# Kernel optimization log

Hardware: AMD Instinct MI355X
Metric: run time of the kernel (lower is better)

Reference implementation:

```python
import jax, jax.numpy as jnp
import numpy as np

H, D = 12, 768
DH = D // H  # 64

def setup_inputs() -> dict:
    key = jax.random.key(0)
    ks = jax.random.split(key, 9)
    s = 0.02
    x  = jax.random.normal(ks[0], (8, 1024, D), dtype=jnp.float32)
    Wq = jax.random.normal(ks[1], (H, D, DH), dtype=jnp.float32) * s
    Wk = jax.random.normal(ks[2], (H, D, DH), dtype=jnp.float32) * s
    Wv = jax.random.normal(ks[3], (H, D, DH), dtype=jnp.float32) * s
    bq = jax.random.normal(ks[4], (H, DH), dtype=jnp.float32) * s
    bk = jax.random.normal(ks[5], (H, DH), dtype=jnp.float32) * s
    bv = jax.random.normal(ks[6], (H, DH), dtype=jnp.float32) * s
    Wo = jax.random.normal(ks[7], (D, D), dtype=jnp.float32) * s
    bo = jax.random.normal(ks[8], (D,), dtype=jnp.float32) * s
    return {"x": x, "Wq": Wq, "Wk": Wk, "Wv": Wv, "bq": bq, "bk": bk, "bv": bv, "Wo": Wo, "bo": bo}

def reference(x, Wq, Wk, Wv, bq, bk, bv, Wo, bo):
    # x: [B,S,D]; per-head projections batched over heads: [B,H,S,DH]
    q = jnp.einsum('bsd,hde->bhse', x, Wq) + bq[None, :, None, :]
    k = jnp.einsum('bsd,hde->bhse', x, Wk) + bk[None, :, None, :]
    v = jnp.einsum('bsd,hde->bhse', x, Wv) + bv[None, :, None, :]
    scores = jnp.einsum('bhse,bhte->bhst', q, k) / jnp.sqrt(jnp.float32(DH))
    probs = jax.nn.softmax(scores, axis=-1)  # dropout is identity (p=0 / eval)
    ctx = jnp.einsum('bhst,bhte->bhse', probs, v)  # [B,H,S,DH]
    B, _, S, _ = ctx.shape
    # concat heads along feature dim (head order matches torch cat order)
    ctx = jnp.transpose(ctx, (0, 2, 1, 3)).reshape(B, S, H * DH)
    out = jnp.einsum('bsd,de->bse', ctx, Wo) + bo
    return out
```

## Files before the change

kernel.cpp:

```cpp
#include <hip/hip_runtime.h>
#include <math.h>


constexpr int NB  = 8;
constexpr int SEQ = 1024;
constexpr int NH  = 12;
constexpr int DM  = 768;
constexpr int DHD = 64;
constexpr int MROWS = NB * SEQ;
constexpr int NQKV  = 3 * NH * DHD;

typedef __attribute__((ext_vector_type(8))) short short8;
typedef __attribute__((ext_vector_type(4))) float f32x4;

#define MFMA16(a,b,c) __builtin_amdgcn_mfma_f32_16x16x32_bf16((a),(b),(c),0,0,0)

#if __has_builtin(__builtin_amdgcn_exp2f)
#define EXP2(x) __builtin_amdgcn_exp2f(x)
#else
#define EXP2(x) exp2f(x)
#endif

__device__ __forceinline__ unsigned short f2bf(float f) {
    unsigned u = __float_as_uint(f);
    return (unsigned short)((u + 0x7fffu + ((u >> 16) & 1u)) >> 16);
}
__device__ __forceinline__ unsigned short f2bf_fast(float f) {
    return (unsigned short)((__float_as_uint(f) + 0x8000u) >> 16);
}

__device__ __forceinline__ void gl_lds16(const unsigned short* g, unsigned short* l) {
    __builtin_amdgcn_global_load_lds(
        (const __attribute__((address_space(1))) void*)g,
        (__attribute__((address_space(3))) void*)l, 16, 0, 0);
}

__device__ __forceinline__ void stageK(unsigned short* lds, const unsigned short* gbase,
                                       int i, int ln, int ldg) {
    int r    = i * 8 + (ln >> 3);
    int cpos = ln & 7;
    int cdat = (cpos - r) & 7;
    gl_lds16(gbase + (size_t)r * ldg + cdat * 8, lds + i * 512);
}
__device__ __forceinline__ short8 ldK(const unsigned short* buf, int row, int chunk) {
    int c = (chunk + row) & 7;
    return *(const short8*)&buf[row * 64 + c * 8];
}

__global__ __launch_bounds__(256) void prep_k(
    const float* __restrict__ x,
    const float* __restrict__ Wq, const float* __restrict__ Wk,
    const float* __restrict__ Wv, const float* __restrict__ Wo,
    unsigned short* __restrict__ xb, unsigned short* __restrict__ wt,
    unsigned short* __restrict__ wot) {
    __shared__ float tb[64][65];
    const int blk = blockIdx.x, tid = threadIdx.x;
    if (blk < 6144) {
        const int i = blk * 256 + tid;
        float4 v = ((const float4*)x)[i];
        ushort4 o;
        o.x = f2bf(v.x); o.y = f2bf(v.y); o.z = f2bf(v.z); o.w = f2bf(v.w);
        ((ushort4*)xb)[i] = o;
        return;
    }
    const int t = blk - 6144;
    const int job = t / 144, lb = t % 144;
    const float* W;
    unsigned short* dst;
    int C, r0, c0;
    if (job < 3) {
        const float* Ws = (job == 0) ? Wq : (job == 1 ? Wk : Wv);
        const int h = lb / 12, rb = lb % 12;
        W = Ws + (size_t)h * (DM * DHD);
        dst = wt + (size_t)(job * 12 + h) * (DM * DHD);
        C = DHD; r0 = rb * 64; c0 = 0;
    } else {
        W = Wo; dst = wot; C = DM;
        r0 = (lb / 12) * 64; c0 = (lb % 12) * 64;
    }
    const int rr = tid >> 2, cc = (tid & 3) * 16;
#pragma unroll
    for (int j = 0; j < 16; j += 4) {
        float4 v = *(const float4*)&W[(size_t)(r0 + rr) * C + c0 + cc + j];
        tb[rr][cc + j + 0] = v.x;
        tb[rr][cc + j + 1] = v.y;
        tb[rr][cc + j + 2] = v.z;
        tb[rr][cc + j + 3] = v.w;
    }
    __syncthreads();
#pragma unroll
    for (int j = 0; j < 16; ++j)
        dst[(size_t)(c0 + rr) * DM + r0 + cc + j] = f2bf(tb[cc + j][rr]);
}

__global__ __launch_bounds__(256, 3) void qkv_mfma_k(
    const unsigned short* __restrict__ xb, const unsigned short* __restrict__ wt,
    const float* __restrict__ bq, const float* __restrict__ bk, const float* __restrict__ bv,
    unsigned short* __restrict__ qb, unsigned short* __restrict__ kb,
    unsigned short* __restrict__ vT) {
    __shared__ unsigned short Ah[128 * 64], Bh[128 * 64];

    const int tid = threadIdx.x;
    const int wv = tid >> 6, ln = tid & 63, quad = ln >> 4, lnid = ln & 15;
    const int wvm = wv >> 1, wvn = wv & 1;
    const int row0 = blockIdx.x * 128, col0 = blockIdx.y * 128;
    const int sel = (col0 >= 2 * DM) ? 2 : (col0 >= DM ? 1 : 0);

    f32x4 acc[4][4];
#pragma unroll
    for (int i = 0; i < 4; ++i)
#pragma unroll
        for (int j = 0; j < 4; ++j) acc[i][j] = (f32x4){0.f, 0.f, 0.f, 0.f};

    const unsigned short* Ahg = xb + (size_t)row0 * DM;
    const unsigned short* Bhg = wt + (size_t)col0 * DM;
    constexpr int NIT = DM / 64;

    if (sel < 2) {
        for (int it = 0; it < NIT; ++it) {
            const int kc = it * 64;
            __syncthreads();
#pragma unroll
            for (int c = 0; c < 4; ++c) {
                stageK(Ah, Ahg + kc, wv * 4 + c, ln, DM);
                stageK(Bh, Bhg + kc, wv * 4 + c, ln, DM);
            }
            __syncthreads();
#pragma unroll
            for (int ks = 0; ks < 2; ++ks) {
                short8 a[4], b[4];
#pragma unroll
                for (int i = 0; i < 4; ++i)
                    a[i] = ldK(Ah, wvm * 64 + i * 16 + lnid, ks * 4 + quad);
#pragma unroll
                for (int j = 0; j < 4; ++j)
                    b[j] = ldK(Bh, wvn * 64 + j * 16 + lnid, ks * 4 + quad);
#pragma unroll
                for (int j = 0; j < 4; ++j)
#pragma unroll
                    for (int i = 0; i < 4; ++i)
                        acc[j][i] = MFMA16(b[j], a[i], acc[j][i]);
            }
        }
        const float scale = (sel == 0) ? 0.18033688011112042f : 1.0f;
        const float* bias = (sel == 0) ? bq : bk;
        unsigned short* oh = (sel == 0) ? qb : kb;
#pragma unroll
        for (int et = 0; et < 4; ++et) {
            const int e = col0 + wvn * 64 + et * 16 + quad * 4;
            const int he = e - sel * DM;
            const int hh2 = he >> 6, ee = he & 63;
            float4 bs = *(const float4*)&bias[he];
#pragma unroll
            for (int st = 0; st < 4; ++st) {
                const int srow = row0 + wvm * 64 + st * 16 + lnid;
                const int bb = srow >> 10, ss = srow & (SEQ - 1);
                ushort4 pk;
                pk.x = f2bf((acc[et][st][0] + bs.x) * scale);
                pk.y = f2bf((acc[et][st][1] + bs.y) * scale);
                pk.z = f2bf((acc[et][st][2] + bs.z) * scale);
                pk.w = f2bf((acc[et][st][3] + bs.w) * scale);
                *(ushort4*)&oh[((size_t)(bb * NH + hh2) * SEQ + ss) * DHD + ee] = pk;
            }
        }
    } else {
        for (int it = 0; it < NIT; ++it) {
            const int kc = it * 64;
            __syncthreads();
#pragma unroll
            for (int c = 0; c < 4; ++c) {
                stageK(Ah, Ahg + kc, wv * 4 + c, ln, DM);
                stageK(Bh, Bhg + kc, wv * 4 + c, ln, DM);
            }
            __syncthreads();
#pragma unroll
            for (int ks = 0; ks < 2; ++ks) {
                short8 a[4], b[4];
#pragma unroll
                for (int i = 0; i < 4; ++i)
                    a[i] = ldK(Ah, wvm * 64 + i * 16 + lnid, ks * 4 + quad);
#pragma unroll
                for (int j = 0; j < 4; ++j)
                    b[j] = ldK(Bh, wvn * 64 + j * 16 + lnid, ks * 4 + quad);
#pragma unroll
                for (int i = 0; i < 4; ++i)
#pragma unroll
                    for (int j = 0; j < 4; ++j)
                        acc[i][j] = MFMA16(a[i], b[j], acc[i][j]);
            }
        }
#pragma unroll
        for (int i = 0; i < 4; ++i) {
#pragma unroll
            for (int j = 0; j < 4; ++j) {
                const int col = col0 + wvn * 64 + j * 16 + lnid;
                const int he = col - 2 * DM;
                const int hh2 = he >> 6, ee = he & 63;
                const float bs = bv[he];
                const int srow = row0 + wvm * 64 + i * 16 + quad * 4;
                const int bb = srow >> 10, ss = srow & (SEQ - 1);
                ushort4 pk;
                pk.x = f2bf(acc[i][j][0] + bs);
                pk.y = f2bf(acc[i][j][1] + bs);
                pk.z = f2bf(acc[i][j][2] + bs);
                pk.w = f2bf(acc[i][j][3] + bs);
                *(ushort4*)&vT[((size_t)(bb * NH + hh2) * DHD + ee) * SEQ + ss] = pk;
            }
        }
    }
}

__global__ __launch_bounds__(512, 6) void attn_mfma_k(
    const unsigned short* __restrict__ qb, const unsigned short* __restrict__ kb,
    const unsigned short* __restrict__ vT, unsigned short* __restrict__ ctb) {
    __shared__ unsigned short ksh[2][64 * 64], vsm[2][64 * 64];
    __shared__ unsigned short ps[128 * 64];

    const int tid = threadIdx.x;
    const int wv = tid >> 6, ln = tid & 63, quad = ln >> 4, lnid = ln & 15;
    const int bhid = blockIdx.x % 96, qt = blockIdx.x / 96;
    const int b = bhid / NH, h = bhid % NH;
    const int q0 = qt * 128;
    const unsigned short* qhb = qb + (size_t)bhid * (SEQ * DHD);
    const unsigned short* khb = kb + (size_t)bhid * (SEQ * DHD);
    const unsigned short* vTb = vT + (size_t)bhid * (DHD * SEQ);

    const int prow = wv * 16 + lnid;

    short8 qf[2];
#pragma unroll
    for (int ks_ = 0; ks_ < 2; ++ks_)
        qf[ks_] = *(const short8*)(qhb + (size_t)(q0 + prow) * DHD + ks_ * 32 + quad * 8);

    f32x4 ctx[4];
#pragma unroll
    for (int j = 0; j < 4; ++j) ctx[j] = (f32x4){0.f, 0.f, 0.f, 0.f};
    float lsum = 0.f;

    stageK(ksh[0], khb, wv, ln, DHD);
    stageK(vsm[0], vTb, wv, ln, SEQ);

    for (int kt = 0; kt < SEQ / 64; ++kt) {
        const int cur = kt & 1;
        __syncthreads();
        if (kt + 1 < SEQ / 64) {
            stageK(ksh[cur ^ 1], khb + (kt + 1) * 64 * DHD, wv, ln, DHD);
            stageK(vsm[cur ^ 1], vTb + (kt + 1) * 64, wv, ln, SEQ);
        }

        f32x4 sc[4];
#pragma unroll
        for (int j = 0; j < 4; ++j) sc[j] = (f32x4){0.f, 0.f, 0.f, 0.f};
#pragma unroll
        for (int ks_ = 0; ks_ < 2; ++ks_) {
#pragma unroll
            for (int nt = 0; nt < 4; ++nt) {
                short8 kf = ldK(ksh[cur], nt * 16 + lnid, ks_ * 4 + quad);
                sc[nt] = MFMA16(kf, qf[ks_], sc[nt]);
            }
        }

#pragma unroll
        for (int nt = 0; nt < 4; ++nt) {
            float p0 = EXP2(sc[nt][0]);
            float p1 = EXP2(sc[nt][1]);
            float p2 = EXP2(sc[nt][2]);
            float p3 = EXP2(sc[nt][3]);
            lsum += (p0 + p1) + (p2 + p3);
            ushort4 pw;
            pw.x = f2bf_fast(p0);
            pw.y = f2bf_fast(p1);
            pw.z = f2bf_fast(p2);
            pw.w = f2bf_fast(p3);
            const int cpos = (2 * nt + (quad >> 1) + prow) & 7;
            *(ushort4*)&ps[prow * 64 + cpos * 8 + (quad & 1) * 4] = pw;
        }

#pragma unroll
        for (int kvs = 0; kvs < 2; ++kvs) {
            short8 pf = ldK(ps, prow, kvs * 4 + quad);
#pragma unroll
            for (int dt = 0; dt < 4; ++dt) {
                short8 vf = ldK(vsm[cur], dt * 16 + lnid, kvs * 4 + quad);
                ctx[dt] = MFMA16(vf, pf, ctx[dt]);
            }
        }
    }

    float s = lsum;
    s += __shfl_xor(s, 16, 64);
    s += __shfl_xor(s, 32, 64);
    const float inv = 1.0f / s;
    const int srow = b * SEQ + q0 + prow;
#pragma unroll
    for (int dt = 0; dt < 4; ++dt) {
        ushort4 pk;
        pk.x = f2bf(ctx[dt][0] * inv);
        pk.y = f2bf(ctx[dt][1] * inv);
        pk.z = f2bf(ctx[dt][2] * inv);
        pk.w = f2bf(ctx[dt][3] * inv);
        *(ushort4*)&ctb[(size_t)srow * DM + h * DHD + dt * 16 + quad * 4] = pk;
    }
}

__global__ __launch_bounds__(256, 3) void out_mfma_k(
    const unsigned short* __restrict__ ctb, const unsigned short* __restrict__ wot,
    const float* __restrict__ bo, float* __restrict__ out) {
    __shared__ unsigned short Ah[128 * 64], Bh[128 * 64];

    const int tid = threadIdx.x;
    const int wv = tid >> 6, ln = tid & 63, quad = ln >> 4, lnid = ln & 15;
    const int wvm = wv >> 1, wvn = wv & 1;
    const int row0 = blockIdx.x * 128, col0 = blockIdx.y * 128;

    f32x4 acc[4][4];
#pragma unroll
    for (int i = 0; i < 4; ++i)
#pragma unroll
        for (int j = 0; j < 4; ++j) acc[i][j] = (f32x4){0.f, 0.f, 0.f, 0.f};

    const unsigned short* Ahg = ctb + (size_t)row0 * DM;
    const unsigned short* Bhg = wot + (size_t)col0 * DM;

    constexpr int NIT = DM / 64;
    for (int it = 0; it < NIT; ++it) {
        const int kc = it * 64;
        __syncthreads();
#pragma unroll
        for (int c = 0; c < 4; ++c) {
            stageK(Ah, Ahg + kc, wv * 4 + c, ln, DM);
            stageK(Bh, Bhg + kc, wv * 4 + c, ln, DM);
        }
        __syncthreads();
#pragma unroll
        for (int ks = 0; ks < 2; ++ks) {
            short8 a[4], b[4];
#pragma unroll
            for (int i = 0; i < 4; ++i)
                a[i] = ldK(Ah, wvm * 64 + i * 16 + lnid, ks * 4 + quad);
#pragma unroll
            for (int j = 0; j < 4; ++j)
                b[j] = ldK(Bh, wvn * 64 + j * 16 + lnid, ks * 4 + quad);
#pragma unroll
            for (int j = 0; j < 4; ++j)
#pragma unroll
                for (int i = 0; i < 4; ++i)
                    acc[j][i] = MFMA16(b[j], a[i], acc[j][i]);
        }
    }

#pragma unroll
    for (int et = 0; et < 4; ++et) {
        const int colb = col0 + wvn * 64 + et * 16 + quad * 4;
        float4 bs = *(const float4*)&bo[colb];
#pragma unroll
        for (int st = 0; st < 4; ++st) {
            const int srow = row0 + wvm * 64 + st * 16 + lnid;
            float4 o;
            o.x = acc[et][st][0] + bs.x;
            o.y = acc[et][st][1] + bs.y;
            o.z = acc[et][st][2] + bs.z;
            o.w = acc[et][st][3] + bs.w;
            *(float4*)&out[(size_t)srow * DM + colb] = o;
        }
    }
}

extern "C" void kernel_launch(void* const* d_in, const int* in_sizes, int n_in,
                              void* d_out, int out_size, void* d_ws, size_t ws_size,
                              hipStream_t stream) {
    const float* x  = (const float*)d_in[0];
    const float* Wq = (const float*)d_in[1];
    const float* Wk = (const float*)d_in[2];
    const float* Wv = (const float*)d_in[3];
    const float* bq = (const float*)d_in[4];
    const float* bk = (const float*)d_in[5];
    const float* bv = (const float*)d_in[6];
    const float* Wo = (const float*)d_in[7];
    const float* bo = (const float*)d_in[8];
    float* out = (float*)d_out;

    char* w = (char*)d_ws;
    const size_t elsX = (size_t)MROWS * DM;
    const size_t elsQ = (size_t)NB * NH * SEQ * DHD;
    unsigned short* xb  = (unsigned short*)w;
    unsigned short* ctb = xb;
    size_t off = elsX * 2;
    unsigned short* wt  = (unsigned short*)(w + off); off += (size_t)NQKV * DM * 2;
    unsigned short* wot = (unsigned short*)(w + off); off += (size_t)DM * DM * 2;
    unsigned short* qbp = (unsigned short*)(w + off); off += elsQ * 2;
    unsigned short* kbp = (unsigned short*)(w + off); off += elsQ * 2;
    unsigned short* vTp = (unsigned short*)(w + off); off += elsQ * 2;

    prep_k<<<dim3(6144 + 576), 256, 0, stream>>>(x, Wq, Wk, Wv, Wo, xb, wt, wot);
    qkv_mfma_k<<<dim3(MROWS / 128, NQKV / 128), 256, 0, stream>>>(
        xb, wt, bq, bk, bv, qbp, kbp, vTp);
    attn_mfma_k<<<dim3(768), 512, 0, stream>>>(qbp, kbp, vTp, ctb);
    out_mfma_k<<<dim3(MROWS / 128, DM / 128), 256, 0, stream>>>(ctb, wot, bo, out);
}
```

Baseline: 190.1 us.

## Use 8-wave blocks in QKV GEMM and prefetch next K tile after fragment reads

The QKV projection kernel now runs 512 threads per block in a 2x4 wave grid, so each wave holds a 64x32 accumulator tile instead of 64x64. The main loop reads the A/B fragments for both k-substeps into registers first, then issues the global loads for the next K chunk into the same LDS buffers while the MFMAs run. This aims to hide global-load latency behind compute and to raise the number of waves per CU. In exchange each wave reuses less data from its fragments, and holding more fragments in registers may add register pressure.

```diff
diff --git a/kernel.cpp b/kernel.cpp
--- a/kernel.cpp
+++ b/kernel.cpp
@@ -93,7 +93,7 @@
         dst[(size_t)(c0 + rr) * DM + r0 + cc + j] = f2bf(tb[cc + j][rr]);
 }
 
-__global__ __launch_bounds__(256, 3) void qkv_mfma_k(
+__global__ __launch_bounds__(512, 4) void qkv_mfma_k(
     const unsigned short* __restrict__ xb, const unsigned short* __restrict__ wt,
     const float* __restrict__ bq, const float* __restrict__ bk, const float* __restrict__ bv,
     unsigned short* __restrict__ qb, unsigned short* __restrict__ kb,
@@ -102,98 +102,118 @@
 
     const int tid = threadIdx.x;
     const int wv = tid >> 6, ln = tid & 63, quad = ln >> 4, lnid = ln & 15;
-    const int wvm = wv >> 1, wvn = wv & 1;
+    const int wvm = wv >> 2, wvn = wv & 3;
     const int row0 = blockIdx.x * 128, col0 = blockIdx.y * 128;
     const int sel = (col0 >= 2 * DM) ? 2 : (col0 >= DM ? 1 : 0);
-
-    f32x4 acc[4][4];
-#pragma unroll
-    for (int i = 0; i < 4; ++i)
-#pragma unroll
-        for (int j = 0; j < 4; ++j) acc[i][j] = (f32x4){0.f, 0.f, 0.f, 0.f};
 
     const unsigned short* Ahg = xb + (size_t)row0 * DM;
     const unsigned short* Bhg = wt + (size_t)col0 * DM;
     constexpr int NIT = DM / 64;
 
+#pragma unroll
+    for (int c = 0; c < 2; ++c) {
+        stageK(Ah, Ahg, wv * 2 + c, ln, DM);
+        stageK(Bh, Bhg, wv * 2 + c, ln, DM);
+    }
+
     if (sel < 2) {
+        f32x4 acc[2][4];
+#pragma unroll
+        for (int j = 0; j < 2; ++j)
+#pragma unroll
+            for (int i = 0; i < 4; ++i) acc[j][i] = (f32x4){0.f, 0.f, 0.f, 0.f};
+
         for (int it = 0; it < NIT; ++it) {
-            const int kc = it * 64;
             __syncthreads();
-#pragma unroll
-            for (int c = 0; c < 4; ++c) {
-                stageK(Ah, Ahg + kc, wv * 4 + c, ln, DM);
-                stageK(Bh, Bhg + kc, wv * 4 + c, ln, DM);
+            short8 a[2][4], b[2][2];
+#pragma unroll
+            for (int ks = 0; ks < 2; ++ks) {
+#pragma unroll
+                for (int i = 0; i < 4; ++i)
+                    a[ks][i] = ldK(Ah, wvm * 64 + i * 16 + lnid, ks * 4 + quad);
+#pragma unroll
+                for (int j = 0; j < 2; ++j)
+                    b[ks][j] = ldK(Bh, wvn * 32 + j * 16 + lnid, ks * 4 + quad);
             }
             __syncthreads();
-#pragma unroll
-            for (int ks = 0; ks < 2; ++ks) {
-                short8 a[4], b[4];
-#pragma unroll
-                for (int i = 0; i < 4; ++i)
-                    a[i] = ldK(Ah, wvm * 64 + i * 16 + lnid, ks * 4 + quad);
-#pragma unroll
-                for (int j = 0; j < 4; ++j)
-                    b[j] = ldK(Bh, wvn * 64 + j * 16 + lnid, ks * 4 + quad);
-#pragma unroll
-                for (int j = 0; j < 4; ++j)
+            if (it + 1 < NIT) {
+                const int kc = (it + 1) * 64;
+#pragma unroll
+                for (int c = 0; c < 2; ++c) {
+                    stageK(Ah, Ahg + kc, wv * 2 + c, ln, DM);
+                    stageK(Bh, Bhg + kc, wv * 2 + c, ln, DM);
+                }
+            }
+#pragma unroll
+            for (int ks = 0; ks < 2; ++ks)
+#pragma unroll
+                for (int j = 0; j < 2; ++j)
 #pragma unroll
                     for (int i = 0; i < 4; ++i)
-                        acc[j][i] = MFMA16(b[j], a[i], acc[j][i]);
-            }
+                        acc[j][i] = MFMA16(b[ks][j], a[ks][i], acc[j][i]);
         }
         const float scale = (sel == 0) ? 0.18033688011112042f : 1.0f;
         const float* bias = (sel == 0) ? bq : bk;
         unsigned short* oh = (sel == 0) ? qb : kb;
 #pragma unroll
-        for (int et = 0; et < 4; ++et) {
-            const int e = col0 + wvn * 64 + et * 16 + quad * 4;
+        for (int jt = 0; jt < 2; ++jt) {
+            const int e = col0 + wvn * 32 + jt * 16 + quad * 4;
             const int he = e - sel * DM;
             const int hh2 = he >> 6, ee = he & 63;
             float4 bs = *(const float4*)&bias[he];
 #pragma unroll
-            for (int st = 0; st < 4; ++st) {
-                const int srow = row0 + wvm * 64 + st * 16 + lnid;
+            for (int it = 0; it < 4; ++it) {
+                const int srow = row0 + wvm * 64 + it * 16 + lnid;
                 const int bb = srow >> 10, ss = srow & (SEQ - 1);
                 ushort4 pk;
-                pk.x = f2bf((acc[et][st][0] + bs.x) * scale);
-                pk.y = f2bf((acc[et][st][1] + bs.y) * scale);
-                pk.z = f2bf((acc[et][st][2] + bs.z) * scale);
-                pk.w = f2bf((acc[et][st][3] + bs.w) * scale);
+                pk.x = f2bf((acc[jt][it][0] + bs.x) * scale);
+                pk.y = f2bf((acc[jt][it][1] + bs.y) * scale);
+                pk.z = f2bf((acc[jt][it][2] + bs.z) * scale);
+                pk.w = f2bf((acc[jt][it][3] + bs.w) * scale);
                 *(ushort4*)&oh[((size_t)(bb * NH + hh2) * SEQ + ss) * DHD + ee] = pk;
             }
         }
     } else {
+        f32x4 acc[4][2];
+#pragma unroll
+        for (int i = 0; i < 4; ++i)
+#pragma unroll
+            for (int j = 0; j < 2; ++j) acc[i][j] = (f32x4){0.f, 0.f, 0.f, 0.f};
+
         for (int it = 0; it < NIT; ++it) {
-            const int kc = it * 64;
             __syncthreads();
-#pragma unroll
-            for (int c = 0; c < 4; ++c) {
-                stageK(Ah, Ahg + kc, wv * 4 + c, ln, DM);
-                stageK(Bh, Bhg + kc, wv * 4 + c, ln, DM);
+            short8 a[2][4], b[2][2];
+#pragma unroll
+            for (int ks = 0; ks < 2; ++ks) {
+#pragma unroll
+                for (int i = 0; i < 4; ++i)
+                    a[ks][i] = ldK(Ah, wvm * 64 + i * 16 + lnid, ks * 4 + quad);
+#pragma unroll
+                for (int j = 0; j < 2; ++j)
+                    b[ks][j] = ldK(Bh, wvn * 32 + j * 16 + lnid, ks * 4 + quad);
             }
             __syncthreads();
-#pragma unroll
-            for (int ks = 0; ks < 2; ++ks) {
-                short8 a[4], b[4];
+            if (it + 1 < NIT) {
+                const int kc = (it + 1) * 64;
+#pragma unroll
+                for (int c = 0; c < 2; ++c) {
+                    stageK(Ah, Ahg + kc, wv * 2 + c, ln, DM);
+                    stageK(Bh, Bhg + kc, wv * 2 + c, ln, DM);
+                }
+            }
+#pragma unroll
+            for (int ks = 0; ks < 2; ++ks)
 #pragma unroll
                 for (int i = 0; i < 4; ++i)
-                    a[i] = ldK(Ah, wvm * 64 + i * 16 + lnid, ks * 4 + quad);
-#pragma unroll
-                for (int j = 0; j < 4; ++j)
-                    b[j] = ldK(Bh, wvn * 64 + j * 16 + lnid, ks * 4 + quad);
-#pragma unroll
-                for (int i = 0; i < 4; ++i)
-#pragma unroll
-                    for (int j = 0; j < 4; ++j)
-                        acc[i][j] = MFMA16(a[i], b[j], acc[i][j]);
-            }
+#pragma unroll
+                    for (int j = 0; j < 2; ++j)
+                        acc[i][j] = MFMA16(a[ks][i], b[ks][j], acc[i][j]);
         }
 #pragma unroll
         for (int i = 0; i < 4; ++i) {
 #pragma unroll
-            for (int j = 0; j < 4; ++j) {
-                const int col = col0 + wvn * 64 + j * 16 + lnid;
+            for (int j = 0; j < 2; ++j) {
+                const int col = col0 + wvn * 32 + j * 16 + lnid;
                 const int he = col - 2 * DM;
                 const int hh2 = he >> 6, ee = he & 63;
                 const float bs = bv[he];
@@ -393,7 +413,7 @@
     unsigned short* vTp = (unsigned short*)(w + off); off += elsQ * 2;
 
     prep_k<<<dim3(6144 + 576), 256, 0, stream>>>(x, Wq, Wk, Wv, Wo, xb, wt, wot);
-    qkv_mfma_k<<<dim3(MROWS / 128, NQKV / 128), 256, 0, stream>>>(
+    qkv_mfma_k<<<dim3(MROWS / 128, NQKV / 128), 512, 0, stream>>>(
         xb, wt, bq, bk, bv, qbp, kbp, vTp);
     attn_mfma_k<<<dim3(768), 512, 0, stream>>>(qbp, kbp, vTp, ctb);
     out_mfma_k<<<dim3(MROWS / 128, DM / 128), 256, 0, stream>>>(ctb, wot, bo, out);
```

Result: slower. 198.4 us (+4.4%).
